# Optimization experiments

Hardware: AMD Instinct MI355X
Metric: run time of the kernel (lower is better)

Reference implementation:

```python
import jax, jax.numpy as jnp
import numpy as np

N_NODES = 100000
N_EDGES = 1600000
NODE_IN = 32
HID = 64
EDGE_IN = 8


def _glorot(key, shape):
    fan_in = shape[0]
    return jax.random.normal(key, shape, jnp.float32) * (1.0 / np.sqrt(fan_in))


def setup_inputs() -> dict:
    key = jax.random.key(0)
    ks = jax.random.split(key, 16)
    d = {}
    d["x"] = jax.random.normal(ks[0], (N_NODES, NODE_IN), jnp.float32)
    d["edge_index"] = jax.random.randint(ks[1], (2, N_EDGES), 0, N_NODES, dtype=jnp.int32)
    d["edge_attr"] = jax.random.normal(ks[2], (N_EDGES, EDGE_IN), jnp.float32)
    # SAGEConv layers: lin_l (aggregated neighbors, with bias), lin_r (root, no bias)
    d["Wl0"] = _glorot(ks[3], (NODE_IN, HID)); d["bl0"] = jnp.zeros((HID,), jnp.float32)
    d["Wr0"] = _glorot(ks[4], (NODE_IN, HID))
    d["Wl1"] = _glorot(ks[5], (HID, HID)); d["bl1"] = jnp.zeros((HID,), jnp.float32)
    d["Wr1"] = _glorot(ks[6], (HID, HID))
    d["Wl2"] = _glorot(ks[7], (HID, HID)); d["bl2"] = jnp.zeros((HID,), jnp.float32)
    d["Wr2"] = _glorot(ks[8], (HID, HID))
    # Edge predictor MLP: (2*HID + EDGE_IN) -> 64 -> 32 -> 1
    pin = 2 * HID + EDGE_IN
    d["W1"] = _glorot(ks[9], (pin, 64)); d["b1"] = jnp.zeros((64,), jnp.float32)
    d["W2"] = _glorot(ks[10], (64, 32)); d["b2"] = jnp.zeros((32,), jnp.float32)
    d["W3"] = _glorot(ks[11], (32, 1)); d["b3"] = jnp.zeros((1,), jnp.float32)
    return d


def _sage_mean(h, src, dst, Wl, bl, Wr):
    # PyG SAGEConv(aggr='mean'): lin_l(mean_{j->i} x_j) + lin_r(x_i)
    n = h.shape[0]
    summed = jax.ops.segment_sum(h[src], dst, num_segments=n)  # [N, F]
    cnt = jax.ops.segment_sum(jnp.ones((src.shape[0], 1), h.dtype), dst, num_segments=n)
    mean = summed / jnp.maximum(cnt, 1.0)
    return mean @ Wl + bl + h @ Wr


def reference(x, edge_index, edge_attr,
              Wl0, bl0, Wr0, Wl1, bl1, Wr1, Wl2, bl2, Wr2,
              W1, b1, W2, b2, W3, b3):
    src, dst = edge_index[0], edge_index[1]
    h = _sage_mean(x, src, dst, Wl0, bl0, Wr0)
    h = jax.nn.relu(h)  # dropout inactive (eval mode)
    h = _sage_mean(h, src, dst, Wl1, bl1, Wr1)
    h = jax.nn.relu(h)
    h = _sage_mean(h, src, dst, Wl2, bl2, Wr2)
    # Edge-level predictor: gather endpoint embeddings + edge features
    edge_repr = jnp.concatenate([h[src], h[dst], edge_attr], axis=1)  # [E, 2*HID+EDGE_IN]
    z = jax.nn.relu(edge_repr @ W1 + b1)
    z = jax.nn.relu(z @ W2 + b2)
    return jax.nn.sigmoid(z @ W3 + b3)  # [E, 1]
```

## Files before the change

kernel.cpp:

```cpp
#include <hip/hip_runtime.h>
#include <hip/hip_bf16.h>

#define NN 100000
#define NE 1600000
#define HID 64
#define SCAN_BS 256
#define NBLK ((NN + SCAN_BS - 1) / SCAN_BS)

typedef float f32x4 __attribute__((ext_vector_type(4)));
typedef short bf16x8 __attribute__((ext_vector_type(8)));

__device__ __forceinline__ float bflo(unsigned u) { return __uint_as_float(u << 16); }
__device__ __forceinline__ float bfhi(unsigned u) { return __uint_as_float(u & 0xffff0000u); }
__device__ __forceinline__ unsigned short f2bf(float f) {
    __hip_bfloat16 h = (__hip_bfloat16)f;
    return *(unsigned short*)&h;
}

__global__ void xcast(const float* __restrict__ in, unsigned short* __restrict__ out, int n4) {
    int i = blockIdx.x * blockDim.x + threadIdx.x;
    if (i >= n4) return;
    float4 v = ((const float4*)in)[i];
    ushort4 o;
    o.x = f2bf(v.x); o.y = f2bf(v.y); o.z = f2bf(v.z); o.w = f2bf(v.w);
    ((ushort4*)out)[i] = o;
}

__global__ void count_kernel(const int* __restrict__ dst, int* __restrict__ degI, int nE) {
    int e = blockIdx.x * blockDim.x + threadIdx.x;
    if (e < nE) atomicAdd(&degI[dst[e]], 1);
}

__global__ void scan1_kernel(const int* __restrict__ degI, int* __restrict__ rowtmp,
                             int* __restrict__ blockSum) {
    __shared__ int tmp[SCAN_BS];
    int t = threadIdx.x;
    int i = blockIdx.x * SCAN_BS + t;
    int d = (i < NN) ? degI[i] : 0;
    tmp[t] = d;
    __syncthreads();
    for (int off = 1; off < SCAN_BS; off <<= 1) {
        int v = (t >= off) ? tmp[t - off] : 0;
        __syncthreads();
        tmp[t] += v;
        __syncthreads();
    }
    if (i < NN) rowtmp[i] = tmp[t] - d;
    if (t == SCAN_BS - 1) blockSum[blockIdx.x] = tmp[t];
}

__global__ void scan2_kernel(const int* __restrict__ blockSum, int* __restrict__ blockOff, int n) {
    __shared__ int tmp[512];
    int t = threadIdx.x;
    tmp[t] = (t < n) ? blockSum[t] : 0;
    __syncthreads();
    for (int off = 1; off < 512; off <<= 1) {
        int v = (t >= off) ? tmp[t - off] : 0;
        __syncthreads();
        tmp[t] += v;
        __syncthreads();
    }
    if (t < n) blockOff[t] = (t == 0) ? 0 : tmp[t - 1];
}

__global__ void scan3_kernel(const int* __restrict__ rowtmp, const int* __restrict__ blockOff,
                             int* __restrict__ row_ptr) {
    int i = blockIdx.x * SCAN_BS + threadIdx.x;
    if (i < NN) row_ptr[i] = rowtmp[i] + blockOff[blockIdx.x];
}

__global__ void fill_kernel(const int* __restrict__ src, const int* __restrict__ dst,
                            const int* __restrict__ row_ptr, int* __restrict__ cursor,
                            int* __restrict__ csr_src, int nE) {
    int e = blockIdx.x * blockDim.x + threadIdx.x;
    if (e >= nE) return;
    int d = dst[e];
    int pos = atomicAdd(&cursor[d], 1);
    csr_src[row_ptr[d] + pos] = src[e];
}

template <int IN>
__launch_bounds__(256)
__global__ void aggregate(const int* __restrict__ row_ptr, const int* __restrict__ degI,
                          const int* __restrict__ csr_src,
                          const unsigned short* __restrict__ hin,
                          float* __restrict__ mout) {
    constexpr int LPE = IN / 8;
    constexpr int SPLIT = 64 / LPE;
    constexpr int UN = (IN == 64) ? 2 : 1;
    int g = threadIdx.x >> 6;
    int lane = threadIdx.x & 63;
    int node = blockIdx.x * 4 + g;
    int lane_p = lane & (LPE - 1);
    int sub = lane / LPE;

    float acc[8];
#pragma unroll
    for (int i = 0; i < 8; ++i) acc[i] = 0.f;

    int start = row_ptr[node];
    int dg = degI[node];
    const int* cs = csr_src + start;

    int e = sub;
    for (; e + SPLIT * (UN - 1) < dg; e += SPLIT * UN) {
        uint4 u[UN];
#pragma unroll
        for (int j = 0; j < UN; ++j) {
            int s = cs[e + SPLIT * j];
            u[j] = *(const uint4*)(hin + (size_t)s * IN + 8 * lane_p);
        }
#pragma unroll
        for (int j = 0; j < UN; ++j) {
            acc[0] += bflo(u[j].x); acc[1] += bfhi(u[j].x);
            acc[2] += bflo(u[j].y); acc[3] += bfhi(u[j].y);
            acc[4] += bflo(u[j].z); acc[5] += bfhi(u[j].z);
            acc[6] += bflo(u[j].w); acc[7] += bfhi(u[j].w);
        }
    }
    for (; e < dg; e += SPLIT) {
        int s = cs[e];
        uint4 u = *(const uint4*)(hin + (size_t)s * IN + 8 * lane_p);
        acc[0] += bflo(u.x); acc[1] += bfhi(u.x);
        acc[2] += bflo(u.y); acc[3] += bfhi(u.y);
        acc[4] += bflo(u.z); acc[5] += bfhi(u.z);
        acc[6] += bflo(u.w); acc[7] += bfhi(u.w);
    }

#pragma unroll
    for (int m = LPE; m < 64; m <<= 1) {
#pragma unroll
        for (int i = 0; i < 8; ++i) acc[i] += __shfl_xor(acc[i], m);
    }
    if (sub == 0) {
        float r = 1.0f / fmaxf((float)dg, 1.0f);
        float4 v0, v1;
        v0.x = acc[0] * r; v0.y = acc[1] * r; v0.z = acc[2] * r; v0.w = acc[3] * r;
        v1.x = acc[4] * r; v1.y = acc[5] * r; v1.z = acc[6] * r; v1.w = acc[7] * r;
        float* p = mout + (size_t)node * IN + 8 * lane_p;
        *(float4*)p = v0;
        *(float4*)(p + 4) = v1;
    }
}

__global__ void wprep(const float* __restrict__ Wl0, const float* __restrict__ Wr0,
                      const float* __restrict__ Wl1, const float* __restrict__ Wr1,
                      const float* __restrict__ Wl2, const float* __restrict__ Wr2,
                      const float* __restrict__ W1, unsigned short* __restrict__ out) {
    int b = blockIdx.x;
    int mid, local;
    if (b < 2) { mid = b; local = 0; }
    else { mid = 2 + (b - 2) / 2; local = (b - 2) & 1; }
    const float* Ws[8] = {Wl0, Wr0, Wl1, Wr1, Wl2, Wr2, W1, W1 + 64 * 64};
    const int offs[8] = {0, 4096, 8192, 16384, 24576, 32768, 40960, 49152};
    const float* W = Ws[mid];
    int e = local * 256 + threadIdx.x;
    int lane = e & 63;
    int fi = e >> 6;
    int ks = fi >> 2, nt = fi & 3;
    int lg = lane >> 4, col = lane & 15;
    unsigned short hi[8], lo[8];
#pragma unroll
    for (int j = 0; j < 8; ++j) {
        float w = W[(ks * 32 + lg * 8 + j) * 64 + nt * 16 + col];
        unsigned short h = f2bf(w);
        hi[j] = h;
        lo[j] = f2bf(w - bflo(h));
    }
    unsigned short* dh = out + offs[mid] + ((size_t)(fi * 2 + 0) * 64 + lane) * 8;
    unsigned short* dl = out + offs[mid] + ((size_t)(fi * 2 + 1) * 64 + lane) * 8;
#pragma unroll
    for (int j = 0; j < 8; ++j) { dh[j] = hi[j]; dl[j] = lo[j]; }
}

template <int KIN, bool RELU>
__launch_bounds__(256)
__global__ void sage_gemm(const float* __restrict__ meanv,
                          const unsigned short* __restrict__ hroot,
                          const unsigned short* __restrict__ wl_pk,
                          const unsigned short* __restrict__ wr_pk,
                          const float* __restrict__ bl,
                          unsigned short* __restrict__ hout) {
    constexpr int NKS = KIN / 32;
    int wid = threadIdx.x >> 6, lane = threadIdx.x & 63;
    int tile = blockIdx.x * 4 + wid;
    if (tile >= NN / 16) return;
    int m0 = tile * 16;
    int ar = lane & 15;
    int lg = lane >> 4;

    bf16x8 ah[NKS];
#pragma unroll
    for (int ks = 0; ks < NKS; ++ks)
        ah[ks] = *(const bf16x8*)(hroot + (size_t)(m0 + ar) * KIN + ks * 32 + lg * 8);

    bf16x8 amh[NKS], aml[NKS];
#pragma unroll
    for (int ks = 0; ks < NKS; ++ks) {
        const float* p = meanv + (size_t)(m0 + ar) * KIN + ks * 32 + lg * 8;
        float4 v0 = *(const float4*)p;
        float4 v1 = *(const float4*)(p + 4);
        float mv[8] = {v0.x, v0.y, v0.z, v0.w, v1.x, v1.y, v1.z, v1.w};
#pragma unroll
        for (int j = 0; j < 8; ++j) {
            unsigned short h = f2bf(mv[j]);
            amh[ks][j] = (short)h;
            aml[ks][j] = (short)f2bf(mv[j] - bflo(h));
        }
    }

#pragma unroll
    for (int nt = 0; nt < 4; ++nt) {
        f32x4 acc = {0.f, 0.f, 0.f, 0.f};
#pragma unroll
        for (int ks = 0; ks < NKS; ++ks) {
            int fi = ks * 4 + nt;
            bf16x8 wlh = *(const bf16x8*)(wl_pk + ((size_t)(fi * 2 + 0) * 64 + lane) * 8);
            bf16x8 wll = *(const bf16x8*)(wl_pk + ((size_t)(fi * 2 + 1) * 64 + lane) * 8);
            bf16x8 wrh = *(const bf16x8*)(wr_pk + ((size_t)(fi * 2 + 0) * 64 + lane) * 8);
            bf16x8 wrl = *(const bf16x8*)(wr_pk + ((size_t)(fi * 2 + 1) * 64 + lane) * 8);
            acc = __builtin_amdgcn_mfma_f32_16x16x32_bf16(amh[ks], wlh, acc, 0, 0, 0);
            acc = __builtin_amdgcn_mfma_f32_16x16x32_bf16(amh[ks], wll, acc, 0, 0, 0);
            acc = __builtin_amdgcn_mfma_f32_16x16x32_bf16(aml[ks], wlh, acc, 0, 0, 0);
            acc = __builtin_amdgcn_mfma_f32_16x16x32_bf16(ah[ks],  wrh, acc, 0, 0, 0);
            acc = __builtin_amdgcn_mfma_f32_16x16x32_bf16(ah[ks],  wrl, acc, 0, 0, 0);
        }
        float b = bl[nt * 16 + ar];
#pragma unroll
        for (int r = 0; r < 4; ++r) {
            float o = acc[r] + b;
            if (RELU) o = fmaxf(o, 0.f);
            hout[(size_t)(m0 + lg * 4 + r) * 64 + nt * 16 + ar] = f2bf(o);
        }
    }
}

__launch_bounds__(256)
__global__ void pred_gemm(const unsigned short* __restrict__ h2,
                          const unsigned short* __restrict__ wa_pk,
                          const unsigned short* __restrict__ wb_pk,
                          unsigned short* __restrict__ a1,
                          unsigned short* __restrict__ a2) {
    int wid = threadIdx.x >> 6, lane = threadIdx.x & 63;
    int tile = blockIdx.x * 4 + wid;
    if (tile >= NN / 16) return;
    int m0 = tile * 16;
    int ar = lane & 15;
    int lg = lane >> 4;
    bf16x8 ah[2];
#pragma unroll
    for (int ks = 0; ks < 2; ++ks)
        ah[ks] = *(const bf16x8*)(h2 + (size_t)(m0 + ar) * 64 + ks * 32 + lg * 8);
#pragma unroll
    for (int nt = 0; nt < 4; ++nt) {
        f32x4 p = {0.f, 0.f, 0.f, 0.f};
        f32x4 q = {0.f, 0.f, 0.f, 0.f};
#pragma unroll
        for (int ks = 0; ks < 2; ++ks) {
            int fi = ks * 4 + nt;
            bf16x8 wah = *(const bf16x8*)(wa_pk + ((size_t)(fi * 2 + 0) * 64 + lane) * 8);
            bf16x8 wal = *(const bf16x8*)(wa_pk + ((size_t)(fi * 2 + 1) * 64 + lane) * 8);
            bf16x8 wbh = *(const bf16x8*)(wb_pk + ((size_t)(fi * 2 + 0) * 64 + lane) * 8);
            bf16x8 wbl = *(const bf16x8*)(wb_pk + ((size_t)(fi * 2 + 1) * 64 + lane) * 8);
            p = __builtin_amdgcn_mfma_f32_16x16x32_bf16(ah[ks], wah, p, 0, 0, 0);
            p = __builtin_amdgcn_mfma_f32_16x16x32_bf16(ah[ks], wal, p, 0, 0, 0);
            q = __builtin_amdgcn_mfma_f32_16x16x32_bf16(ah[ks], wbh, q, 0, 0, 0);
            q = __builtin_amdgcn_mfma_f32_16x16x32_bf16(ah[ks], wbl, q, 0, 0, 0);
        }
#pragma unroll
        for (int r = 0; r < 4; ++r) {
            size_t off = (size_t)(m0 + lg * 4 + r) * 64 + nt * 16 + ar;
            a1[off] = f2bf(p[r]);
            a2[off] = f2bf(q[r]);
        }
    }
}

__launch_bounds__(256)
__global__ void edge_pred(const int* __restrict__ src, const int* __restrict__ dst,
                          const unsigned short* __restrict__ a1, const unsigned short* __restrict__ a2,
                          const float* __restrict__ ea,
                          const float* __restrict__ W1, const float* __restrict__ b1,
                          const float* __restrict__ W2, const float* __restrict__ b2,
                          const float* __restrict__ W3, const float* __restrict__ b3,
                          float* __restrict__ out, int nE) {
    int e = blockIdx.x * blockDim.x + threadIdx.x;
    if (e >= nE) return;
    int s = src[e];
    int d = dst[e];

    const uint4* pa = (const uint4*)(a1 + (size_t)s * 64);
    const uint4* pb = (const uint4*)(a2 + (size_t)d * 64);
    const float4* eav = (const float4*)(ea + (size_t)e * 8);
    float4 v0 = eav[0];
    float4 v1 = eav[1];

    float z1[64];
    const float* wr = W1 + 128 * 64;
#pragma unroll
    for (int j = 0; j < 64; ++j) {
        float a = fmaf(v0.x, wr[j], b1[j]);
        a = fmaf(v0.y, wr[64 + j], a);
        a = fmaf(v0.z, wr[128 + j], a);
        a = fmaf(v0.w, wr[192 + j], a);
        a = fmaf(v1.x, wr[256 + j], a);
        a = fmaf(v1.y, wr[320 + j], a);
        a = fmaf(v1.z, wr[384 + j], a);
        z1[j] = fmaf(v1.w, wr[448 + j], a);
    }

#pragma unroll
    for (int q = 0; q < 8; ++q) {
        uint4 ua = pa[q];
        uint4 ub = pb[q];
        int j0 = q * 8;
        z1[j0 + 0] += bflo(ua.x) + bflo(ub.x);
        z1[j0 + 1] += bfhi(ua.x) + bfhi(ub.x);
        z1[j0 + 2] += bflo(ua.y) + bflo(ub.y);
        z1[j0 + 3] += bfhi(ua.y) + bfhi(ub.y);
        z1[j0 + 4] += bflo(ua.z) + bflo(ub.z);
        z1[j0 + 5] += bfhi(ua.z) + bfhi(ub.z);
        z1[j0 + 6] += bflo(ua.w) + bflo(ub.w);
        z1[j0 + 7] += bfhi(ua.w) + bfhi(ub.w);
    }

    float z2[32];
#pragma unroll
    for (int j = 0; j < 32; ++j) z2[j] = b2[j];
    for (int k = 0; k < 64; ++k) {
        float v = fmaxf(z1[k], 0.0f);
        const float* w = W2 + (size_t)k * 32;
#pragma unroll
        for (int j = 0; j < 32; ++j) z2[j] = fmaf(v, w[j], z2[j]);
    }

    float o = b3[0];
#pragma unroll
    for (int k = 0; k < 32; ++k) o = fmaf(fmaxf(z2[k], 0.0f), W3[k], o);

    out[e] = 1.0f / (1.0f + __expf(-o));
}

extern "C" void kernel_launch(void* const* d_in, const int* in_sizes, int n_in,
                              void* d_out, int out_size, void* d_ws, size_t ws_size,
                              hipStream_t stream) {
    const float* x   = (const float*)d_in[0];
    const int*   ei  = (const int*)d_in[1];
    const float* ea  = (const float*)d_in[2];
    const float* Wl0 = (const float*)d_in[3];
    const float* bl0 = (const float*)d_in[4];
    const float* Wr0 = (const float*)d_in[5];
    const float* Wl1 = (const float*)d_in[6];
    const float* bl1 = (const float*)d_in[7];
    const float* Wr1 = (const float*)d_in[8];
    const float* Wl2 = (const float*)d_in[9];
    const float* bl2 = (const float*)d_in[10];
    const float* Wr2 = (const float*)d_in[11];
    const float* W1  = (const float*)d_in[12];
    const float* b1  = (const float*)d_in[13];
    const float* W2  = (const float*)d_in[14];
    const float* b2  = (const float*)d_in[15];
    const float* W3  = (const float*)d_in[16];
    const float* b3  = (const float*)d_in[17];

    const int* src = ei;
    const int* dst = ei + NE;

    char* ws = (char*)d_ws;
    size_t off = 0;
    auto alloc = [&](size_t bytes) {
        void* p = ws + off;
        off += (bytes + 255) & ~(size_t)255;
        return p;
    };
    unsigned short* xb = (unsigned short*)alloc((size_t)NN * 32 * 2);
    unsigned short* hA = (unsigned short*)alloc((size_t)NN * HID * 2);
    unsigned short* hB = (unsigned short*)alloc((size_t)NN * HID * 2);
    unsigned short* a1 = (unsigned short*)alloc((size_t)NN * HID * 2);
    unsigned short* a2 = (unsigned short*)alloc((size_t)NN * HID * 2);
    unsigned short* wpk = (unsigned short*)alloc((size_t)57344 * 2);
    int* degI    = (int*)alloc(NN * sizeof(int));
    int* row_ptr = (int*)alloc(NN * sizeof(int));
    int* rowtmp  = (int*)alloc(NN * sizeof(int));
    int* cursor  = (int*)alloc(NN * sizeof(int));
    int* blockSum= (int*)alloc(512 * sizeof(int));
    int* blockOff= (int*)alloc(512 * sizeof(int));
    int* csr_src = (int*)alloc((size_t)NE * sizeof(int));
    float* meanv = (float*)a1;
    float* out = (float*)d_out;

    const int BS = 256;
    dim3 blkE((NE + BS - 1) / BS);
    int n4 = NN * 32 / 4;
    int gemm_blk = (NN / 16 + 3) / 4;

    hipMemsetAsync(degI, 0, NN * sizeof(int), stream);
    hipMemsetAsync(cursor, 0, NN * sizeof(int), stream);
    xcast<<<(n4 + BS - 1) / BS, BS, 0, stream>>>(x, xb, n4);
    count_kernel<<<blkE, BS, 0, stream>>>(dst, degI, NE);
    scan1_kernel<<<NBLK, SCAN_BS, 0, stream>>>(degI, rowtmp, blockSum);
    scan2_kernel<<<1, 512, 0, stream>>>(blockSum, blockOff, NBLK);
    scan3_kernel<<<NBLK, SCAN_BS, 0, stream>>>(rowtmp, blockOff, row_ptr);
    fill_kernel<<<blkE, BS, 0, stream>>>(src, dst, row_ptr, cursor, csr_src, NE);
    wprep<<<14, 256, 0, stream>>>(Wl0, Wr0, Wl1, Wr1, Wl2, Wr2, W1, wpk);

    aggregate<32><<<NN / 4, 256, 0, stream>>>(row_ptr, degI, csr_src, xb, meanv);
    sage_gemm<32, true><<<gemm_blk, 256, 0, stream>>>(meanv, xb, wpk + 0, wpk + 4096, bl0, hA);
    aggregate<64><<<NN / 4, 256, 0, stream>>>(row_ptr, degI, csr_src, hA, meanv);
    sage_gemm<64, true><<<gemm_blk, 256, 0, stream>>>(meanv, hA, wpk + 8192, wpk + 16384, bl1, hB);
    aggregate<64><<<NN / 4, 256, 0, stream>>>(row_ptr, degI, csr_src, hB, meanv);
    sage_gemm<64, false><<<gemm_blk, 256, 0, stream>>>(meanv, hB, wpk + 24576, wpk + 32768, bl2, hA);
    pred_gemm<<<gemm_blk, 256, 0, stream>>>(hA, wpk + 40960, wpk + 49152, a1, a2);

    edge_pred<<<blkE, BS, 0, stream>>>(src, dst, a1, a2, ea, W1, b1, W2, b2, W3, b3, out, NE);
}
```

Baseline: 556.5 us.

## Fuse neighbor aggregation with SAGE GEMM and predictor GEMM per tile

Each SAGE layer now gathers and averages neighbors for a 16-node tile inside the GEMM kernel, keeping the means in LDS instead of writing an fp32 mean buffer to global memory and reading it back. The last layer also runs the edge-predictor projection in the same kernel using an LDS staging tile. This drops four kernel launches and the mean round-trip. In exchange, one wave now loops serially over 16 nodes, which cuts the number of independent waves available for the gather phase and may reduce latency hiding.

```diff
diff --git a/kernel.cpp b/kernel.cpp
--- a/kernel.cpp
+++ b/kernel.cpp
@@ -6,6 +6,7 @@
 #define HID 64
 #define SCAN_BS 256
 #define NBLK ((NN + SCAN_BS - 1) / SCAN_BS)
+#define NTILE (NN / 16)
 
 typedef float f32x4 __attribute__((ext_vector_type(4)));
 typedef short bf16x8 __attribute__((ext_vector_type(8)));
@@ -77,70 +78,6 @@
     int d = dst[e];
     int pos = atomicAdd(&cursor[d], 1);
     csr_src[row_ptr[d] + pos] = src[e];
-}
-
-template <int IN>
-__launch_bounds__(256)
-__global__ void aggregate(const int* __restrict__ row_ptr, const int* __restrict__ degI,
-                          const int* __restrict__ csr_src,
-                          const unsigned short* __restrict__ hin,
-                          float* __restrict__ mout) {
-    constexpr int LPE = IN / 8;
-    constexpr int SPLIT = 64 / LPE;
-    constexpr int UN = (IN == 64) ? 2 : 1;
-    int g = threadIdx.x >> 6;
-    int lane = threadIdx.x & 63;
-    int node = blockIdx.x * 4 + g;
-    int lane_p = lane & (LPE - 1);
-    int sub = lane / LPE;
-
-    float acc[8];
-#pragma unroll
-    for (int i = 0; i < 8; ++i) acc[i] = 0.f;
-
-    int start = row_ptr[node];
-    int dg = degI[node];
-    const int* cs = csr_src + start;
-
-    int e = sub;
-    for (; e + SPLIT * (UN - 1) < dg; e += SPLIT * UN) {
-        uint4 u[UN];
-#pragma unroll
-        for (int j = 0; j < UN; ++j) {
-            int s = cs[e + SPLIT * j];
-            u[j] = *(const uint4*)(hin + (size_t)s * IN + 8 * lane_p);
-        }
-#pragma unroll
-        for (int j = 0; j < UN; ++j) {
-            acc[0] += bflo(u[j].x); acc[1] += bfhi(u[j].x);
-            acc[2] += bflo(u[j].y); acc[3] += bfhi(u[j].y);
-            acc[4] += bflo(u[j].z); acc[5] += bfhi(u[j].z);
-            acc[6] += bflo(u[j].w); acc[7] += bfhi(u[j].w);
-        }
-    }
-    for (; e < dg; e += SPLIT) {
-        int s = cs[e];
-        uint4 u = *(const uint4*)(hin + (size_t)s * IN + 8 * lane_p);
-        acc[0] += bflo(u.x); acc[1] += bfhi(u.x);
-        acc[2] += bflo(u.y); acc[3] += bfhi(u.y);
-        acc[4] += bflo(u.z); acc[5] += bfhi(u.z);
-        acc[6] += bflo(u.w); acc[7] += bfhi(u.w);
-    }
-
-#pragma unroll
-    for (int m = LPE; m < 64; m <<= 1) {
-#pragma unroll
-        for (int i = 0; i < 8; ++i) acc[i] += __shfl_xor(acc[i], m);
-    }
-    if (sub == 0) {
-        float r = 1.0f / fmaxf((float)dg, 1.0f);
-        float4 v0, v1;
-        v0.x = acc[0] * r; v0.y = acc[1] * r; v0.z = acc[2] * r; v0.w = acc[3] * r;
-        v1.x = acc[4] * r; v1.y = acc[5] * r; v1.z = acc[6] * r; v1.w = acc[7] * r;
-        float* p = mout + (size_t)node * IN + 8 * lane_p;
-        *(float4*)p = v0;
-        *(float4*)(p + 4) = v1;
-    }
 }
 
 __global__ void wprep(const float* __restrict__ Wl0, const float* __restrict__ Wr0,
@@ -173,31 +110,98 @@
     for (int j = 0; j < 8; ++j) { dh[j] = hi[j]; dl[j] = lo[j]; }
 }
 
-template <int KIN, bool RELU>
+template <int IN, bool RELU, bool LAST>
 __launch_bounds__(256)
-__global__ void sage_gemm(const float* __restrict__ meanv,
-                          const unsigned short* __restrict__ hroot,
-                          const unsigned short* __restrict__ wl_pk,
-                          const unsigned short* __restrict__ wr_pk,
-                          const float* __restrict__ bl,
-                          unsigned short* __restrict__ hout) {
-    constexpr int NKS = KIN / 32;
+__global__ void sage_fused(const int* __restrict__ row_ptr, const int* __restrict__ degI,
+                           const int* __restrict__ csr_src,
+                           const unsigned short* __restrict__ hin,
+                           const unsigned short* __restrict__ wl_pk,
+                           const unsigned short* __restrict__ wr_pk,
+                           const float* __restrict__ bl,
+                           unsigned short* __restrict__ hout,
+                           const unsigned short* __restrict__ wa_pk,
+                           const unsigned short* __restrict__ wb_pk,
+                           unsigned short* __restrict__ a1,
+                           unsigned short* __restrict__ a2) {
+    constexpr int NKS = IN / 32;
+    constexpr int LPE = IN / 8;
+    constexpr int SPLIT = 64 / LPE;
+    constexpr int LDW = IN + 4;
+
+    __shared__ float meanL[4][16][LDW];
+
     int wid = threadIdx.x >> 6, lane = threadIdx.x & 63;
     int tile = blockIdx.x * 4 + wid;
-    if (tile >= NN / 16) return;
+    if (tile >= NTILE) tile = NTILE - 1;
     int m0 = tile * 16;
-    int ar = lane & 15;
-    int lg = lane >> 4;
+    int ar = lane & 15, lg = lane >> 4;
+    int lane_p = lane & (LPE - 1);
+    int sub = lane / LPE;
+
+    int start0 = 0, deg0 = 0;
+    if (lane < 16) { start0 = row_ptr[m0 + lane]; deg0 = degI[m0 + lane]; }
+
+    float (*ml)[LDW] = meanL[wid];
+
+    for (int i = 0; i < 16; ++i) {
+        int st = __shfl(start0, i);
+        int dg = __shfl(deg0, i);
+        const int* cs = csr_src + st;
+
+        float acc[8];
+#pragma unroll
+        for (int k = 0; k < 8; ++k) acc[k] = 0.f;
+
+        int e = sub;
+        for (; e + SPLIT < dg; e += SPLIT * 2) {
+            int s0 = cs[e];
+            int s1 = cs[e + SPLIT];
+            uint4 u0 = *(const uint4*)(hin + (size_t)s0 * IN + 8 * lane_p);
+            uint4 u1 = *(const uint4*)(hin + (size_t)s1 * IN + 8 * lane_p);
+            acc[0] += bflo(u0.x); acc[1] += bfhi(u0.x);
+            acc[2] += bflo(u0.y); acc[3] += bfhi(u0.y);
+            acc[4] += bflo(u0.z); acc[5] += bfhi(u0.z);
+            acc[6] += bflo(u0.w); acc[7] += bfhi(u0.w);
+            acc[0] += bflo(u1.x); acc[1] += bfhi(u1.x);
+            acc[2] += bflo(u1.y); acc[3] += bfhi(u1.y);
+            acc[4] += bflo(u1.z); acc[5] += bfhi(u1.z);
+            acc[6] += bflo(u1.w); acc[7] += bfhi(u1.w);
+        }
+        for (; e < dg; e += SPLIT) {
+            int s = cs[e];
+            uint4 u = *(const uint4*)(hin + (size_t)s * IN + 8 * lane_p);
+            acc[0] += bflo(u.x); acc[1] += bfhi(u.x);
+            acc[2] += bflo(u.y); acc[3] += bfhi(u.y);
+            acc[4] += bflo(u.z); acc[5] += bfhi(u.z);
+            acc[6] += bflo(u.w); acc[7] += bfhi(u.w);
+        }
+
+#pragma unroll
+        for (int m = LPE; m < 64; m <<= 1) {
+#pragma unroll
+            for (int k = 0; k < 8; ++k) acc[k] += __shfl_xor(acc[k], m);
+        }
+        if (sub == 0) {
+            float r = 1.0f / fmaxf((float)dg, 1.0f);
+            float* p = &ml[i][8 * lane_p];
+            float4 v0, v1;
+            v0.x = acc[0] * r; v0.y = acc[1] * r; v0.z = acc[2] * r; v0.w = acc[3] * r;
+            v1.x = acc[4] * r; v1.y = acc[5] * r; v1.z = acc[6] * r; v1.w = acc[7] * r;
+            *(float4*)p = v0;
+            *(float4*)(p + 4) = v1;
+        }
+    }
+    __syncthreads();
 
     bf16x8 ah[NKS];
 #pragma unroll
     for (int ks = 0; ks < NKS; ++ks)
-        ah[ks] = *(const bf16x8*)(hroot + (size_t)(m0 + ar) * KIN + ks * 32 + lg * 8);
+        ah[ks] = *(const bf16x8*)(hin + (size_t)(m0 + ar) * IN + ks * 32 + lg * 8);
 
     bf16x8 amh[NKS], aml[NKS];
 #pragma unroll
     for (int ks = 0; ks < NKS; ++ks) {
-        const float* p = meanv + (size_t)(m0 + ar) * KIN + ks * 32 + lg * 8;
+        const float* p = &ml[ar][ks * 32 + lg * 8];
         float4 v0 = *(const float4*)p;
         float4 v1 = *(const float4*)(p + 4);
         float mv[8] = {v0.x, v0.y, v0.z, v0.w, v1.x, v1.y, v1.z, v1.w};
@@ -209,6 +213,7 @@
         }
     }
 
+    f32x4 accv[4];
 #pragma unroll
     for (int nt = 0; nt < 4; ++nt) {
         f32x4 acc = {0.f, 0.f, 0.f, 0.f};
@@ -225,53 +230,58 @@
             acc = __builtin_amdgcn_mfma_f32_16x16x32_bf16(ah[ks],  wrh, acc, 0, 0, 0);
             acc = __builtin_amdgcn_mfma_f32_16x16x32_bf16(ah[ks],  wrl, acc, 0, 0, 0);
         }
-        float b = bl[nt * 16 + ar];
-#pragma unroll
-        for (int r = 0; r < 4; ++r) {
-            float o = acc[r] + b;
-            if (RELU) o = fmaxf(o, 0.f);
-            hout[(size_t)(m0 + lg * 4 + r) * 64 + nt * 16 + ar] = f2bf(o);
-        }
-    }
-}
-
-__launch_bounds__(256)
-__global__ void pred_gemm(const unsigned short* __restrict__ h2,
-                          const unsigned short* __restrict__ wa_pk,
-                          const unsigned short* __restrict__ wb_pk,
-                          unsigned short* __restrict__ a1,
-                          unsigned short* __restrict__ a2) {
-    int wid = threadIdx.x >> 6, lane = threadIdx.x & 63;
-    int tile = blockIdx.x * 4 + wid;
-    if (tile >= NN / 16) return;
-    int m0 = tile * 16;
-    int ar = lane & 15;
-    int lg = lane >> 4;
-    bf16x8 ah[2];
-#pragma unroll
-    for (int ks = 0; ks < 2; ++ks)
-        ah[ks] = *(const bf16x8*)(h2 + (size_t)(m0 + ar) * 64 + ks * 32 + lg * 8);
-#pragma unroll
-    for (int nt = 0; nt < 4; ++nt) {
-        f32x4 p = {0.f, 0.f, 0.f, 0.f};
-        f32x4 q = {0.f, 0.f, 0.f, 0.f};
-#pragma unroll
-        for (int ks = 0; ks < 2; ++ks) {
-            int fi = ks * 4 + nt;
-            bf16x8 wah = *(const bf16x8*)(wa_pk + ((size_t)(fi * 2 + 0) * 64 + lane) * 8);
-            bf16x8 wal = *(const bf16x8*)(wa_pk + ((size_t)(fi * 2 + 1) * 64 + lane) * 8);
-            bf16x8 wbh = *(const bf16x8*)(wb_pk + ((size_t)(fi * 2 + 0) * 64 + lane) * 8);
-            bf16x8 wbl = *(const bf16x8*)(wb_pk + ((size_t)(fi * 2 + 1) * 64 + lane) * 8);
-            p = __builtin_amdgcn_mfma_f32_16x16x32_bf16(ah[ks], wah, p, 0, 0, 0);
-            p = __builtin_amdgcn_mfma_f32_16x16x32_bf16(ah[ks], wal, p, 0, 0, 0);
-            q = __builtin_amdgcn_mfma_f32_16x16x32_bf16(ah[ks], wbh, q, 0, 0, 0);
-            q = __builtin_amdgcn_mfma_f32_16x16x32_bf16(ah[ks], wbl, q, 0, 0, 0);
-        }
-#pragma unroll
-        for (int r = 0; r < 4; ++r) {
-            size_t off = (size_t)(m0 + lg * 4 + r) * 64 + nt * 16 + ar;
-            a1[off] = f2bf(p[r]);
-            a2[off] = f2bf(q[r]);
+        accv[nt] = acc;
+    }
+
+    if constexpr (!LAST) {
+#pragma unroll
+        for (int nt = 0; nt < 4; ++nt) {
+            float b = bl[nt * 16 + ar];
+#pragma unroll
+            for (int r = 0; r < 4; ++r) {
+                float o = accv[nt][r] + b;
+                if (RELU) o = fmaxf(o, 0.f);
+                hout[(size_t)(m0 + lg * 4 + r) * 64 + nt * 16 + ar] = f2bf(o);
+            }
+        }
+    } else {
+        __shared__ unsigned short h2L[4][16][72];
+#pragma unroll
+        for (int nt = 0; nt < 4; ++nt) {
+            float b = bl[nt * 16 + ar];
+#pragma unroll
+            for (int r = 0; r < 4; ++r)
+                h2L[wid][lg * 4 + r][nt * 16 + ar] = f2bf(accv[nt][r] + b);
+        }
+        __syncthreads();
+
+        bf16x8 h2f[2];
+#pragma unroll
+        for (int ks = 0; ks < 2; ++ks)
+            h2f[ks] = *(const bf16x8*)(&h2L[wid][ar][ks * 32 + lg * 8]);
+
+#pragma unroll
+        for (int nt = 0; nt < 4; ++nt) {
+            f32x4 p = {0.f, 0.f, 0.f, 0.f};
+            f32x4 q = {0.f, 0.f, 0.f, 0.f};
+#pragma unroll
+            for (int ks = 0; ks < 2; ++ks) {
+                int fi = ks * 4 + nt;
+                bf16x8 wah = *(const bf16x8*)(wa_pk + ((size_t)(fi * 2 + 0) * 64 + lane) * 8);
+                bf16x8 wal = *(const bf16x8*)(wa_pk + ((size_t)(fi * 2 + 1) * 64 + lane) * 8);
+                bf16x8 wbh = *(const bf16x8*)(wb_pk + ((size_t)(fi * 2 + 0) * 64 + lane) * 8);
+                bf16x8 wbl = *(const bf16x8*)(wb_pk + ((size_t)(fi * 2 + 1) * 64 + lane) * 8);
+                p = __builtin_amdgcn_mfma_f32_16x16x32_bf16(h2f[ks], wah, p, 0, 0, 0);
+                p = __builtin_amdgcn_mfma_f32_16x16x32_bf16(h2f[ks], wal, p, 0, 0, 0);
+                q = __builtin_amdgcn_mfma_f32_16x16x32_bf16(h2f[ks], wbh, q, 0, 0, 0);
+                q = __builtin_amdgcn_mfma_f32_16x16x32_bf16(h2f[ks], wbl, q, 0, 0, 0);
+            }
+#pragma unroll
+            for (int r = 0; r < 4; ++r) {
+                size_t off = (size_t)(m0 + lg * 4 + r) * 64 + nt * 16 + ar;
+                a1[off] = f2bf(p[r]);
+                a2[off] = f2bf(q[r]);
+            }
         }
     }
 }
@@ -386,13 +396,12 @@
     int* blockSum= (int*)alloc(512 * sizeof(int));
     int* blockOff= (int*)alloc(512 * sizeof(int));
     int* csr_src = (int*)alloc((size_t)NE * sizeof(int));
-    float* meanv = (float*)a1;
     float* out = (float*)d_out;
 
     const int BS = 256;
     dim3 blkE((NE + BS - 1) / BS);
     int n4 = NN * 32 / 4;
-    int gemm_blk = (NN / 16 + 3) / 4;
+    int fused_blk = (NTILE + 3) / 4;
 
     hipMemsetAsync(degI, 0, NN * sizeof(int), stream);
     hipMemsetAsync(cursor, 0, NN * sizeof(int), stream);
@@ -404,13 +413,15 @@
     fill_kernel<<<blkE, BS, 0, stream>>>(src, dst, row_ptr, cursor, csr_src, NE);
     wprep<<<14, 256, 0, stream>>>(Wl0, Wr0, Wl1, Wr1, Wl2, Wr2, W1, wpk);
 
-    aggregate<32><<<NN / 4, 256, 0, stream>>>(row_ptr, degI, csr_src, xb, meanv);
-    sage_gemm<32, true><<<gemm_blk, 256, 0, stream>>>(meanv, xb, wpk + 0, wpk + 4096, bl0, hA);
-    aggregate<64><<<NN / 4, 256, 0, stream>>>(row_ptr, degI, csr_src, hA, meanv);
-    sage_gemm<64, true><<<gemm_blk, 256, 0, stream>>>(meanv, hA, wpk + 8192, wpk + 16384, bl1, hB);
-    aggregate<64><<<NN / 4, 256, 0, stream>>>(row_ptr, degI, csr_src, hB, meanv);
-    sage_gemm<64, false><<<gemm_blk, 256, 0, stream>>>(meanv, hB, wpk + 24576, wpk + 32768, bl2, hA);
-    pred_gemm<<<gemm_blk, 256, 0, stream>>>(hA, wpk + 40960, wpk + 49152, a1, a2);
+    sage_fused<32, true,  false><<<fused_blk, 256, 0, stream>>>(
+        row_ptr, degI, csr_src, xb, wpk + 0, wpk + 4096, bl0, hA,
+        nullptr, nullptr, nullptr, nullptr);
+    sage_fused<64, true,  false><<<fused_blk, 256, 0, stream>>>(
+        row_ptr, degI, csr_src, hA, wpk + 8192, wpk + 16384, bl1, hB,
+        nullptr, nullptr, nullptr, nullptr);
+    sage_fused<64, false, true ><<<fused_blk, 256, 0, stream>>>(
+        row_ptr, degI, csr_src, hB, wpk + 24576, wpk + 32768, bl2, nullptr,
+        wpk + 40960, wpk + 49152, a1, a2);
 
     edge_pred<<<blkE, BS, 0, stream>>>(src, dst, a1, a2, ea, W1, b1, W2, b2, W3, b3, out, NE);
 }
```

Measured after the change: 585.0 us. 1.05x slower.
